# Performance work log

Measured on AMD Instinct MI355X. Metric: run time of the kernel, lower is better.

Reference implementation:

```python
import jax, jax.numpy as jnp
import numpy as np

N = 100000
NFEAT = 512
NHID = 256
NCLASS = 40
E = 1600000
K = 10          # nlayers propagation hops
ALPHA = 0.1


def setup_inputs() -> dict:
    key = jax.random.key(0)
    ks = jax.random.split(key, 8)
    x = jax.random.normal(ks[0], (N, NFEAT), dtype=jnp.float32)
    edge_src = jax.random.randint(ks[1], (E,), 0, N, dtype=jnp.int32)
    edge_dst = jax.random.randint(ks[2], (E,), 0, N, dtype=jnp.int32)
    # roughly row-stochastic-scale edge values (avg degree ~16)
    edge_val = jax.random.uniform(ks[3], (E,), dtype=jnp.float32) * (1.0 / 16.0)
    stdv1 = 1.0 / np.sqrt(NFEAT)
    W1 = jax.random.uniform(ks[4], (NFEAT, NHID), minval=-stdv1, maxval=stdv1, dtype=jnp.float32)
    b1 = jax.random.uniform(ks[5], (NHID,), minval=-stdv1, maxval=stdv1, dtype=jnp.float32)
    stdv2 = 1.0 / np.sqrt(NHID)
    W2 = jax.random.uniform(ks[6], (NHID, NCLASS), minval=-stdv2, maxval=stdv2, dtype=jnp.float32)
    b2 = jax.random.uniform(ks[7], (NCLASS,), minval=-stdv2, maxval=stdv2, dtype=jnp.float32)
    return {"x": x, "edge_src": edge_src, "edge_dst": edge_dst, "edge_val": edge_val,
            "W1": W1, "b1": b1, "W2": W2, "b2": b2}


def _spmm(edge_src, edge_dst, edge_val, z):
    # sparse adj @ z via gather + segment-sum scatter: out[dst] += val * z[src]
    msgs = edge_val[:, None] * z[edge_src]          # [E, C]
    return jax.ops.segment_sum(msgs, edge_dst, num_segments=N)


def reference(x, edge_src, edge_dst, edge_val, W1, b1, W2, b2):
    # MLP transform (dropout is identity in eval mode)
    h = jax.nn.relu(x @ W1 + b1)                    # [N, NHID]
    h = h @ W2 + b2                                 # [N, NCLASS]
    # APPNP propagation: z <- (1-alpha) * A z + alpha * h
    def step(z, _):
        z = _spmm(edge_src, edge_dst, edge_val, z) * (1.0 - ALPHA) + ALPHA * h
        return z, None
    z, _ = jax.lax.scan(step, h, None, length=K)
    return jax.nn.log_softmax(z, axis=1)
```

## Files before the change

### kernel.cpp

```cpp
#include <hip/hip_runtime.h>
#include <hip/hip_bf16.h>
#include <math.h>

#define NN     100000
#define NFEATD 512
#define NHIDD  256
#define NCLS   40
#define NE     1600000
#define KHOP   10

typedef __attribute__((ext_vector_type(8))) short short8;
typedef __attribute__((ext_vector_type(4))) float floatx4;

static __device__ __forceinline__ float bf2f(unsigned int u) {
  unsigned int x = u << 16;
  float f;
  __builtin_memcpy(&f, &x, 4);
  return f;
}
static __device__ __forceinline__ unsigned short f2bf(float f) {
  unsigned int x;
  __builtin_memcpy(&x, &f, 4);
  x = (x + 0x7fffu + ((x >> 16) & 1u)) >> 16;
  return (unsigned short)x;
}
static __device__ __forceinline__ void bf8_to_f(const uint4 u, float* f) {
  unsigned int a0 = u.x, a1 = u.y, a2 = u.z, a3 = u.w;
  unsigned int t;
  t = a0 << 16;          __builtin_memcpy(&f[0], &t, 4);
  t = a0 & 0xffff0000u;  __builtin_memcpy(&f[1], &t, 4);
  t = a1 << 16;          __builtin_memcpy(&f[2], &t, 4);
  t = a1 & 0xffff0000u;  __builtin_memcpy(&f[3], &t, 4);
  t = a2 << 16;          __builtin_memcpy(&f[4], &t, 4);
  t = a2 & 0xffff0000u;  __builtin_memcpy(&f[5], &t, 4);
  t = a3 << 16;          __builtin_memcpy(&f[6], &t, 4);
  t = a3 & 0xffff0000u;  __builtin_memcpy(&f[7], &t, 4);
}

__global__ __launch_bounds__(256) void wt_kernel(const float* __restrict__ W1,
                                                 unsigned short* __restrict__ Wt) {
  int i = blockIdx.x * 256 + threadIdx.x;
  int k = i >> 8;
  int n = i & 255;
  Wt[n * 512 + k] = f2bf(W1[i]);
}

__global__ __launch_bounds__(256) void gemm1_mfma_kernel(
    const float* __restrict__ x, const unsigned short* __restrict__ Wt,
    const float* __restrict__ b1, unsigned short* __restrict__ h1) {
  __shared__ __align__(16) unsigned short smem_u[20480];
  unsigned short* As0 = smem_u;
  unsigned short* Bs0 = smem_u + 5120;
  unsigned short* As1 = smem_u + 10240;
  unsigned short* Bs1 = smem_u + 15360;
  unsigned short* hs = smem_u;
  const int tid = threadIdx.x;
  const int lane = tid & 63;
  const int wave = tid >> 6;
  const int wr = wave >> 1, wc = wave & 1;
  const int m = lane & 15, quad = lane >> 4;
  const int c0 = blockIdx.x * 128;
  const int r0 = blockIdx.y * 128;

  const int arow = tid >> 3;
  const int akq = tid & 7;
  const int brow = tid >> 2;
  const int bkq = tid & 3;

  floatx4 acc[4][4];
#pragma unroll
  for (int i = 0; i < 4; ++i)
#pragma unroll
    for (int j = 0; j < 4; ++j) acc[i][j] = (floatx4){0.f, 0.f, 0.f, 0.f};

  const float* asrc[4];
#pragma unroll
  for (int rep = 0; rep < 4; ++rep) {
    int grow = r0 + arow + rep * 32;
    asrc[rep] = x + (size_t)(grow < NN ? grow : 0) * NFEATD + akq * 4;
  }
  const unsigned short* bsrc[2];
#pragma unroll
  for (int rep = 0; rep < 2; ++rep)
    bsrc[rep] = Wt + (size_t)(c0 + brow + rep * 64) * NFEATD + bkq * 8;

#define LOAD_A(dst, koff)                                        \
  {                                                              \
    _Pragma("unroll") for (int rep = 0; rep < 4; ++rep)          \
        dst[rep] = *(const float4*)(asrc[rep] + (koff));         \
  }
#define LOAD_B(dst, koff)                                        \
  {                                                              \
    _Pragma("unroll") for (int rep = 0; rep < 2; ++rep)          \
        dst[rep] = *(const uint4*)(bsrc[rep] + (koff));          \
  }
#define STAGE(Ad, Bd, aregs, bregs)                              \
  {                                                              \
    _Pragma("unroll") for (int rep = 0; rep < 4; ++rep) {        \
      ushort4 o;                                                 \
      o.x = f2bf(aregs[rep].x);                                  \
      o.y = f2bf(aregs[rep].y);                                  \
      o.z = f2bf(aregs[rep].z);                                  \
      o.w = f2bf(aregs[rep].w);                                  \
      *(ushort4*)&Ad[(arow + rep * 32) * 40 + akq * 4] = o;      \
    }                                                            \
    _Pragma("unroll") for (int rep = 0; rep < 2; ++rep)          \
        *(uint4*)&Bd[(brow + rep * 64) * 40 + bkq * 8] = bregs[rep]; \
  }
#define COMPUTE(Asb, Bsb)                                        \
  {                                                              \
    short8 af[4], bfr[4];                                        \
    _Pragma("unroll") for (int i = 0; i < 4; ++i)                \
        af[i] = *(const short8*)&Asb[(wr * 64 + i * 16 + m) * 40 + quad * 8]; \
    _Pragma("unroll") for (int j = 0; j < 4; ++j)                \
        bfr[j] = *(const short8*)&Bsb[(wc * 64 + j * 16 + m) * 40 + quad * 8]; \
    _Pragma("unroll") for (int i = 0; i < 4; ++i)                \
        _Pragma("unroll") for (int j = 0; j < 4; ++j)            \
            acc[i][j] = __builtin_amdgcn_mfma_f32_16x16x32_bf16( \
                af[i], bfr[j], acc[i][j], 0, 0, 0);              \
  }
#define BAR()                                                    \
  {                                                              \
    asm volatile("s_waitcnt lgkmcnt(0)" ::: "memory");           \
    __builtin_amdgcn_s_barrier();                                \
  }

  float4 aA[4];
  uint4 bA[2];
  LOAD_A(aA, 0); LOAD_B(bA, 0);
  STAGE(As0, Bs0, aA, bA);
  LOAD_A(aA, 32); LOAD_B(bA, 32);
  BAR();

#pragma unroll 1
  for (int t = 0; t < 8; ++t) {
    const int kt = t * 64;
    STAGE(As1, Bs1, aA, bA);
    if (t < 7) { LOAD_A(aA, kt + 64); LOAD_B(bA, kt + 64); }
    COMPUTE(As0, Bs0);
    BAR();
    if (t < 7) {
      STAGE(As0, Bs0, aA, bA);
      LOAD_A(aA, kt + 96); LOAD_B(bA, kt + 96);
    }
    COMPUTE(As1, Bs1);
    BAR();
  }

  float bias[4];
#pragma unroll
  for (int j = 0; j < 4; ++j) bias[j] = b1[c0 + wc * 64 + j * 16 + m];
#pragma unroll
  for (int i = 0; i < 4; ++i)
#pragma unroll
    for (int r = 0; r < 4; ++r) {
      int rl = wr * 64 + i * 16 + quad * 4 + r;
#pragma unroll
      for (int j = 0; j < 4; ++j)
        hs[rl * 128 + wc * 64 + j * 16 + m] =
            f2bf(fmaxf(acc[i][j][r] + bias[j], 0.f));
    }
  BAR();
#pragma unroll
  for (int rep = 0; rep < 8; ++rep) {
    int idx = rep * 256 + tid;
    int row = idx >> 4;
    int grow = r0 + row;
    if (grow < NN) {
      uint4 v = *(const uint4*)&hs[idx * 8];
      *(uint4*)(h1 + (size_t)grow * NHIDD + c0 + (idx & 15) * 8) = v;
    }
  }
#undef LOAD_A
#undef LOAD_B
#undef STAGE
#undef COMPUTE
#undef BAR
}

__global__ __launch_bounds__(256) void gemm2_kernel(
    const unsigned short* __restrict__ h1, const float* __restrict__ W2,
    const float* __restrict__ b2, unsigned short* __restrict__ hb) {
  __shared__ float w2s[NHIDD * NCLS];
  __shared__ float b2s[NCLS];
  __shared__ unsigned short h1s[64 * 264];
  const int tid = threadIdx.x;
  const int r0 = blockIdx.x * 64;
#pragma unroll
  for (int i = 0; i < 10; ++i)
    ((float4*)w2s)[tid + i * 256] = ((const float4*)W2)[tid + i * 256];
  if (tid < NCLS) b2s[tid] = b2[tid];
#pragma unroll
  for (int q = 0; q < 8; ++q) {
    int l = tid + q * 256;
    int lr = l >> 5;
    int lc = (l & 31) << 3;
    int row = r0 + lr;
    uint4 v = make_uint4(0, 0, 0, 0);
    if (row < NN) v = *(const uint4*)(h1 + (size_t)row * NHIDD + lc);
    *(uint4*)&h1s[lr * 264 + lc] = v;
  }
  __syncthreads();
  const int lr = tid >> 2;
  const int cq = (tid & 3) * 10;
  float acc[10];
#pragma unroll
  for (int j = 0; j < 10; ++j) acc[j] = 0.f;
#pragma unroll 4
  for (int k = 0; k < NHIDD; k += 2) {
    unsigned int hp = *(const unsigned int*)&h1s[lr * 264 + k];
    float a0 = bf2f(hp & 0xffffu);
    float a1 = bf2f(hp >> 16);
    const float* w0 = &w2s[k * NCLS + cq];
    const float* w1 = &w2s[(k + 1) * NCLS + cq];
#pragma unroll
    for (int j2 = 0; j2 < 5; ++j2) {
      float2 wa = *(const float2*)(w0 + 2 * j2);
      float2 wb = *(const float2*)(w1 + 2 * j2);
      acc[2 * j2] = fmaf(a1, wb.x, fmaf(a0, wa.x, acc[2 * j2]));
      acc[2 * j2 + 1] = fmaf(a1, wb.y, fmaf(a0, wa.y, acc[2 * j2 + 1]));
    }
  }
  int row = r0 + lr;
  if (row < NN) {
#pragma unroll
    for (int jj = 0; jj < 5; ++jj) {
      unsigned int u = (unsigned int)f2bf(acc[2 * jj] + b2s[cq + 2 * jj]) |
                       ((unsigned int)f2bf(acc[2 * jj + 1] + b2s[cq + 2 * jj + 1]) << 16);
      *(unsigned int*)&hb[(size_t)row * NCLS + cq + 2 * jj] = u;
    }
  }
}

__global__ __launch_bounds__(256) void zero_kernel(int* __restrict__ p, int n) {
  int i = blockIdx.x * 256 + threadIdx.x;
  if (i < n) p[i] = 0;
}
__global__ __launch_bounds__(256) void count_kernel(const int* __restrict__ edst,
                                                    int* __restrict__ counts) {
  int e = blockIdx.x * 256 + threadIdx.x;
  if (e < NE) atomicAdd(&counts[edst[e]], 1);
}
__global__ __launch_bounds__(256) void hist_kernel(const int* __restrict__ counts,
                                                   int* __restrict__ binoff) {
  __shared__ int lhist[64];
  int tid = threadIdx.x;
  if (tid < 64) lhist[tid] = 0;
  __syncthreads();
  int r = blockIdx.x * 256 + tid;
  if (r < NN) {
    int d = counts[r];
    if (d > 63) d = 63;
    atomicAdd(&lhist[d], 1);
  }
  __syncthreads();
  if (tid < 64) {
    int c = lhist[tid];
    if (c) atomicAdd(&binoff[tid], c);
  }
}
__global__ __launch_bounds__(64) void binscan_kernel(int* __restrict__ binoff) {
  __shared__ int s[64];
  int t = threadIdx.x;
  s[t] = binoff[t];
  __syncthreads();
  if (t == 0) {
    int run = 0;
    for (int i = 0; i < 64; ++i) {
      int c = s[i];
      s[i] = run;
      run += c;
    }
  }
  __syncthreads();
  binoff[t] = s[t];
}
__global__ __launch_bounds__(256) void scatter_rows_kernel(
    const int* __restrict__ counts, int* __restrict__ binoff,
    int* __restrict__ perm, int* __restrict__ spos) {
  __shared__ int lhist[64];
  __shared__ int lbase[64];
  int tid = threadIdx.x;
  if (tid < 64) lhist[tid] = 0;
  __syncthreads();
  int r = blockIdx.x * 256 + tid;
  int d = 0, lrank = 0;
  bool valid = (r < NN);
  if (valid) {
    d = counts[r];
    if (d > 63) d = 63;
    lrank = atomicAdd(&lhist[d], 1);
  }
  __syncthreads();
  if (tid < 64) {
    int c = lhist[tid];
    lbase[tid] = c ? atomicAdd(&binoff[tid], c) : 0;
  }
  __syncthreads();
  if (valid) {
    int pos = lbase[d] + lrank;
    perm[pos] = r;
    spos[r] = pos;
  }
}
__global__ __launch_bounds__(256) void scan_blocks_kernel(
    const int* __restrict__ counts, const int* __restrict__ perm,
    int* __restrict__ srs, int* __restrict__ bsum) {
  __shared__ int s[256];
  int gid = blockIdx.x * 256 + threadIdx.x;
  int v = (gid < NN) ? counts[perm[gid]] : 0;
  s[threadIdx.x] = v;
  __syncthreads();
  for (int off = 1; off < 256; off <<= 1) {
    int t = (threadIdx.x >= off) ? s[threadIdx.x - off] : 0;
    __syncthreads();
    s[threadIdx.x] += t;
    __syncthreads();
  }
  if (gid < NN) srs[gid + 1] = s[threadIdx.x];
  if (threadIdx.x == 255) bsum[blockIdx.x] = s[255];
}
#define NB 391
__global__ __launch_bounds__(512) void scan_sums_kernel(int* __restrict__ bsum) {
  __shared__ int s[512];
  int tid = threadIdx.x;
  int v = (tid < NB) ? bsum[tid] : 0;
  s[tid] = v;
  __syncthreads();
  for (int off = 1; off < 512; off <<= 1) {
    int t = (tid >= off) ? s[tid - off] : 0;
    __syncthreads();
    s[tid] += t;
    __syncthreads();
  }
  if (tid < NB) bsum[tid] = (tid == 0) ? 0 : s[tid - 1];
}
__global__ __launch_bounds__(256) void add_off_kernel(int* __restrict__ srs,
                                                      const int* __restrict__ bsum) {
  int gid = blockIdx.x * 256 + threadIdx.x;
  if (gid < NN) srs[gid + 1] += bsum[blockIdx.x];
  if (gid == 0) srs[0] = 0;
}
__global__ __launch_bounds__(256) void scatter_kernel(
    const int* __restrict__ esrc, const int* __restrict__ edst,
    const float* __restrict__ eval, const int* __restrict__ srs,
    const int* __restrict__ spos, int* __restrict__ cursor,
    int2* __restrict__ csr_pair) {
  int e = blockIdx.x * 256 + threadIdx.x;
  if (e < NE) {
    int p = spos[edst[e]];
    int idx = srs[p] + atomicAdd(&cursor[p], 1);
    csr_pair[idx] = make_int2(esrc[e], __float_as_int(eval[e]));
  }
}

__global__ __launch_bounds__(256) void prop_kernel(
    const int* __restrict__ srs, const int* __restrict__ perm,
    const int2* __restrict__ csr_pair, const unsigned short* __restrict__ zi,
    const unsigned short* __restrict__ hb, unsigned short* __restrict__ zo) {
  int t = blockIdx.x * 256 + threadIdx.x;
  if (t >= NN * 5) return;
  unsigned int p = (unsigned int)t / 5u;
  int cg8 = (t - (int)p * 5) * 8;
  int e0 = srs[p], e1 = srs[p + 1];
  int r = perm[p];
  float acc[8];
#pragma unroll
  for (int j = 0; j < 8; ++j) acc[j] = 0.f;

  int e = e0;
  for (; e + 8 <= e1; e += 8) {
    int2 pr[8];
#pragma unroll
    for (int q = 0; q < 8; ++q) pr[q] = csr_pair[e + q];
    uint4 g[8];
#pragma unroll
    for (int q = 0; q < 8; ++q)
      g[q] = *(const uint4*)(zi + pr[q].x * NCLS + cg8);
#pragma unroll
    for (int q = 0; q < 8; ++q) {
      float zf[8];
      bf8_to_f(g[q], zf);
      float v = __int_as_float(pr[q].y);
#pragma unroll
      for (int j = 0; j < 8; ++j) acc[j] = fmaf(v, zf[j], acc[j]);
    }
  }
  for (; e < e1; ++e) {
    int2 pr = csr_pair[e];
    uint4 g = *(const uint4*)(zi + pr.x * NCLS + cg8);
    float zf[8];
    bf8_to_f(g, zf);
    float v = __int_as_float(pr.y);
#pragma unroll
    for (int j = 0; j < 8; ++j) acc[j] = fmaf(v, zf[j], acc[j]);
  }

  uint4 hu = *(const uint4*)(hb + r * NCLS + cg8);
  float hf[8];
  bf8_to_f(hu, hf);
  uint4 o;
  unsigned int wv[4];
#pragma unroll
  for (int i = 0; i < 4; ++i) {
    unsigned int lo = f2bf(0.9f * acc[2 * i] + 0.1f * hf[2 * i]);
    unsigned int hi = f2bf(0.9f * acc[2 * i + 1] + 0.1f * hf[2 * i + 1]);
    wv[i] = lo | (hi << 16);
  }
  o.x = wv[0];
  o.y = wv[1];
  o.z = wv[2];
  o.w = wv[3];
  *(uint4*)(zo + r * NCLS + cg8) = o;
}

__global__ __launch_bounds__(256) void lsm_kernel(const unsigned short* __restrict__ zf,
                                                  float* __restrict__ out) {
  int r = blockIdx.x * 256 + threadIdx.x;
  if (r >= NN) return;
  float v[NCLS];
#pragma unroll
  for (int q = 0; q < 5; ++q) {
    uint4 u = *(const uint4*)(zf + r * NCLS + q * 8);
    bf8_to_f(u, v + q * 8);
  }
  float m = v[0];
#pragma unroll
  for (int i = 1; i < NCLS; ++i) m = fmaxf(m, v[i]);
  float ssum = 0.f;
#pragma unroll
  for (int i = 0; i < NCLS; ++i) ssum += expf(v[i] - m);
  float lse = m + logf(ssum);
#pragma unroll
  for (int q = 0; q < 10; ++q) {
    float4 o;
    o.x = v[q * 4 + 0] - lse;
    o.y = v[q * 4 + 1] - lse;
    o.z = v[q * 4 + 2] - lse;
    o.w = v[q * 4 + 3] - lse;
    *(float4*)(out + r * NCLS + q * 4) = o;
  }
}

extern "C" void kernel_launch(void* const* d_in, const int* in_sizes, int n_in,
                              void* d_out, int out_size, void* d_ws, size_t ws_size,
                              hipStream_t stream) {
  const float* x = (const float*)d_in[0];
  const int* esrc = (const int*)d_in[1];
  const int* edst = (const int*)d_in[2];
  const float* eval = (const float*)d_in[3];
  const float* W1 = (const float*)d_in[4];
  const float* b1 = (const float*)d_in[5];
  const float* W2 = (const float*)d_in[6];
  const float* b2 = (const float*)d_in[7];
  float* out = (float*)d_out;
  char* ws = (char*)d_ws;

  unsigned short* hb = (unsigned short*)(ws + 0);
  unsigned short* zB0 = (unsigned short*)(ws + 8000000);
  unsigned short* zB1 = (unsigned short*)(ws + 16000000);
  unsigned short* Wt = (unsigned short*)(ws + 24000000);
  unsigned short* h1 = (unsigned short*)(ws + 24400000);
  int* counts = (int*)(ws + 75600000);
  int* cursor = (int*)(ws + 76000000);
  int* srs = (int*)(ws + 76400000);
  int* bsum = (int*)(ws + 76800064);
  int* binoff = (int*)(ws + 76802112);
  int* perm = (int*)(ws + 76802624);
  int* spos = (int*)(ws + 77202624);
  int2* csr_pair = (int2*)(ws + 77602624);

  zero_kernel<<<(2 * NN + 255) / 256, 256, 0, stream>>>(counts, 2 * NN);
  zero_kernel<<<1, 256, 0, stream>>>(binoff, 64);

  wt_kernel<<<(NFEATD * NHIDD) / 256, 256, 0, stream>>>(W1, Wt);
  gemm1_mfma_kernel<<<dim3(2, (NN + 127) / 128), 256, 0, stream>>>(x, Wt, b1, h1);
  gemm2_kernel<<<(NN + 63) / 64, 256, 0, stream>>>(h1, W2, b2, hb);

  count_kernel<<<(NE + 255) / 256, 256, 0, stream>>>(edst, counts);
  hist_kernel<<<(NN + 255) / 256, 256, 0, stream>>>(counts, binoff);
  binscan_kernel<<<1, 64, 0, stream>>>(binoff);
  scatter_rows_kernel<<<(NN + 255) / 256, 256, 0, stream>>>(counts, binoff, perm, spos);
  scan_blocks_kernel<<<NB, 256, 0, stream>>>(counts, perm, srs, bsum);
  scan_sums_kernel<<<1, 512, 0, stream>>>(bsum);
  add_off_kernel<<<NB, 256, 0, stream>>>(srs, bsum);
  scatter_kernel<<<(NE + 255) / 256, 256, 0, stream>>>(esrc, edst, eval, srs, spos,
                                                       cursor, csr_pair);

  const unsigned short* zin = hb;
  unsigned short* zout = zB0;
  for (int i = 0; i < KHOP; ++i) {
    prop_kernel<<<(NN * 5 + 255) / 256, 256, 0, stream>>>(srs, perm, csr_pair,
                                                          zin, hb, zout);
    if (i == 0) {
      zin = zB0;
      zout = zB1;
    } else {
      unsigned short* t = (unsigned short*)zin;
      zin = zout;
      zout = t;
    }
  }

  lsm_kernel<<<(NN + 255) / 256, 256, 0, stream>>>(zB1, out);
}
```

Baseline: 1.037 ms.

## Stage block edge ranges in shared memory for propagation SpMM

The propagation kernel now gives each block 48 consecutive sorted rows, spread as 12 rows per wave with 5 lanes per row. Each block loads its contiguous CSR edge pairs into LDS in chunks of 2048, and the threads then gather z rows using indices read from LDS. This removes the repeated global loads of each edge pair by the 5 column-group threads and makes those loads coalesced. The cost is block-wide barriers, 4 of 64 lanes idle in every wave, and waves that sit waiting on the longest row in the block.

```diff
diff --git a/kernel.cpp b/kernel.cpp
--- a/kernel.cpp
+++ b/kernel.cpp
@@ -354,64 +354,103 @@
   }
 }
 
+#define PROWS 48
+#define ECHUNK 2048
 __global__ __launch_bounds__(256) void prop_kernel(
     const int* __restrict__ srs, const int* __restrict__ perm,
     const int2* __restrict__ csr_pair, const unsigned short* __restrict__ zi,
     const unsigned short* __restrict__ hb, unsigned short* __restrict__ zo) {
-  int t = blockIdx.x * 256 + threadIdx.x;
-  if (t >= NN * 5) return;
-  unsigned int p = (unsigned int)t / 5u;
-  int cg8 = (t - (int)p * 5) * 8;
-  int e0 = srs[p], e1 = srs[p + 1];
-  int r = perm[p];
+  __shared__ int2 epairs[ECHUNK];
+  const int tid = threadIdx.x;
+  const int lane = tid & 63;
+  const int wave = tid >> 6;
+  const int rw = lane / 5;
+  const int g = lane - rw * 5;
+  const int p_base = blockIdx.x * PROWS;
+  const int p = p_base + wave * 12 + rw;
+  const bool active = (lane < 60) && (rw < 12) && (p < NN);
+  int pend = p_base + PROWS;
+  if (pend > NN) pend = NN;
+  const int eb = srs[p_base];
+  const int ee = srs[pend];
+  int e0 = 0, e1 = 0, r = 0;
+  if (active) {
+    e0 = srs[p];
+    e1 = srs[p + 1];
+    r = perm[p];
+  }
+  const int cg8 = g * 8;
   float acc[8];
 #pragma unroll
   for (int j = 0; j < 8; ++j) acc[j] = 0.f;
 
-  int e = e0;
-  for (; e + 8 <= e1; e += 8) {
-    int2 pr[8];
-#pragma unroll
-    for (int q = 0; q < 8; ++q) pr[q] = csr_pair[e + q];
-    uint4 g[8];
-#pragma unroll
-    for (int q = 0; q < 8; ++q)
-      g[q] = *(const uint4*)(zi + pr[q].x * NCLS + cg8);
-#pragma unroll
-    for (int q = 0; q < 8; ++q) {
-      float zf[8];
-      bf8_to_f(g[q], zf);
-      float v = __int_as_float(pr[q].y);
-#pragma unroll
-      for (int j = 0; j < 8; ++j) acc[j] = fmaf(v, zf[j], acc[j]);
-    }
-  }
-  for (; e < e1; ++e) {
-    int2 pr = csr_pair[e];
-    uint4 g = *(const uint4*)(zi + pr.x * NCLS + cg8);
-    float zf[8];
-    bf8_to_f(g, zf);
-    float v = __int_as_float(pr.y);
-#pragma unroll
-    for (int j = 0; j < 8; ++j) acc[j] = fmaf(v, zf[j], acc[j]);
-  }
-
-  uint4 hu = *(const uint4*)(hb + r * NCLS + cg8);
-  float hf[8];
-  bf8_to_f(hu, hf);
-  uint4 o;
-  unsigned int wv[4];
-#pragma unroll
-  for (int i = 0; i < 4; ++i) {
-    unsigned int lo = f2bf(0.9f * acc[2 * i] + 0.1f * hf[2 * i]);
-    unsigned int hi = f2bf(0.9f * acc[2 * i + 1] + 0.1f * hf[2 * i + 1]);
-    wv[i] = lo | (hi << 16);
-  }
-  o.x = wv[0];
-  o.y = wv[1];
-  o.z = wv[2];
-  o.w = wv[3];
-  *(uint4*)(zo + r * NCLS + cg8) = o;
+  for (int cb = eb; cb < ee; cb += ECHUNK) {
+    int cnt = ee - cb;
+    if (cnt > ECHUNK) cnt = ECHUNK;
+    __syncthreads();
+    for (int i = tid; i < cnt; i += 256) epairs[i] = csr_pair[cb + i];
+    __syncthreads();
+    if (active) {
+      int s = e0 > cb ? e0 : cb;
+      int t_ = e1 < cb + cnt ? e1 : cb + cnt;
+      int e = s;
+      for (; e + 4 <= t_; e += 4) {
+        int2 pr0 = epairs[e - cb];
+        int2 pr1 = epairs[e - cb + 1];
+        int2 pr2 = epairs[e - cb + 2];
+        int2 pr3 = epairs[e - cb + 3];
+        uint4 g0 = *(const uint4*)(zi + (size_t)pr0.x * NCLS + cg8);
+        uint4 g1 = *(const uint4*)(zi + (size_t)pr1.x * NCLS + cg8);
+        uint4 g2 = *(const uint4*)(zi + (size_t)pr2.x * NCLS + cg8);
+        uint4 g3 = *(const uint4*)(zi + (size_t)pr3.x * NCLS + cg8);
+        float zf[8];
+        bf8_to_f(g0, zf);
+        float v0 = __int_as_float(pr0.y);
+#pragma unroll
+        for (int j = 0; j < 8; ++j) acc[j] = fmaf(v0, zf[j], acc[j]);
+        bf8_to_f(g1, zf);
+        float v1 = __int_as_float(pr1.y);
+#pragma unroll
+        for (int j = 0; j < 8; ++j) acc[j] = fmaf(v1, zf[j], acc[j]);
+        bf8_to_f(g2, zf);
+        float v2 = __int_as_float(pr2.y);
+#pragma unroll
+        for (int j = 0; j < 8; ++j) acc[j] = fmaf(v2, zf[j], acc[j]);
+        bf8_to_f(g3, zf);
+        float v3 = __int_as_float(pr3.y);
+#pragma unroll
+        for (int j = 0; j < 8; ++j) acc[j] = fmaf(v3, zf[j], acc[j]);
+      }
+      for (; e < t_; ++e) {
+        int2 pr = epairs[e - cb];
+        uint4 gq = *(const uint4*)(zi + (size_t)pr.x * NCLS + cg8);
+        float zf[8];
+        bf8_to_f(gq, zf);
+        float v = __int_as_float(pr.y);
+#pragma unroll
+        for (int j = 0; j < 8; ++j) acc[j] = fmaf(v, zf[j], acc[j]);
+      }
+    }
+  }
+
+  if (active) {
+    uint4 hu = *(const uint4*)(hb + (size_t)r * NCLS + cg8);
+    float hf[8];
+    bf8_to_f(hu, hf);
+    uint4 o;
+    unsigned int wv[4];
+#pragma unroll
+    for (int i = 0; i < 4; ++i) {
+      unsigned int lo = f2bf(0.9f * acc[2 * i] + 0.1f * hf[2 * i]);
+      unsigned int hi = f2bf(0.9f * acc[2 * i + 1] + 0.1f * hf[2 * i + 1]);
+      wv[i] = lo | (hi << 16);
+    }
+    o.x = wv[0];
+    o.y = wv[1];
+    o.z = wv[2];
+    o.w = wv[3];
+    *(uint4*)(zo + (size_t)r * NCLS + cg8) = o;
+  }
 }
 
 __global__ __launch_bounds__(256) void lsm_kernel(const unsigned short* __restrict__ zf,
@@ -490,8 +529,8 @@
   const unsigned short* zin = hb;
   unsigned short* zout = zB0;
   for (int i = 0; i < KHOP; ++i) {
-    prop_kernel<<<(NN * 5 + 255) / 256, 256, 0, stream>>>(srs, perm, csr_pair,
-                                                          zin, hb, zout);
+    prop_kernel<<<(NN + PROWS - 1) / PROWS, 256, 0, stream>>>(srs, perm, csr_pair,
+                                                              zin, hb, zout);
     if (i == 0) {
       zin = zB0;
       zout = zB1;
```

New measurement: 960.8 us. 1.08x faster.
